# Kernel tuning notes

Hardware: AMD Instinct MI355X
Metric: run time of the kernel (lower is better)

The kernel has to match this reference:

```python
import jax, jax.numpy as jnp
import numpy as np

X_DIM, R_DIM, U_DIM, V_DIM, H_DIM = 64, 64, 64, 64, 128


def setup_inputs() -> dict:
    key = jax.random.key(0)
    k1, k2, k3, k4, k5 = jax.random.split(key, 5)
    n, i, j = 8, 32, 32
    r = jax.random.normal(k1, (n, i, j, R_DIM), dtype=jnp.float32)
    u = jax.random.normal(k2, (n, R_DIM, U_DIM, V_DIM), dtype=jnp.float32)
    v = jax.random.normal(k3, (n, i, j, V_DIM), dtype=jnp.float32)
    # xavier_uniform scaling: gain=1, fan computed over last two dims per torch default
    def xavier(k, shape):
        fan_in, fan_out = shape[-1], shape[-2]
        # torch xavier on >2D tensor: fan_in = shape[1]*prod(shape[2:]), fan_out = shape[0]*prod(shape[2:])
        rf = int(np.prod(shape[2:])) if len(shape) > 2 else 1
        fi = shape[1] * rf
        fo = shape[0] * rf
        bound = float(np.sqrt(6.0 / (fi + fo)))
        return jax.random.uniform(k, shape, dtype=jnp.float32, minval=-bound, maxval=bound)
    w1 = xavier(k4, (R_DIM, U_DIM, V_DIM, H_DIM))
    w2 = xavier(k5, (X_DIM, R_DIM, H_DIM))
    return {"r": r, "u": u, "v": v, "w1": w1, "w2": w2}


def reference(r, u, v, w1, w2):
    # contract w1 with u over (u_dim, v_dim) -> per-batch tensor a[n, r, v', h]
    # original: einsum('ruvh,nruv,nijv->nijrh')
    a = jnp.einsum('ruvh,nruv->nrvh', w1, u)          # contract u axis; v survives? no:
    # Careful: in 'ruvh,nruv,nijv->nijrh', v is contracted across all three.
    # Do it in two GEMM-friendly steps: first contract u-axis, keeping v.
    # a: [n, r, v, h] (contracted only over u)
    a = jnp.einsum('ruvh,nruv->nrvh', w1, u)
    # then contract v with v-tensor: [n,i,j,v] x [n,r,v,h] -> [n,i,j,r,h]
    x = jax.nn.relu(jnp.einsum('nijv,nrvh->nijrh', v, a))
    # second einsum: 'xrh,nijr,nijrh->nijx'
    # fuse r-weighting into x first (elementwise over r), then contract (r,h) with w2
    out = jnp.einsum('xrh,nijrh->nijx', w2, x * r[..., None])
    return out
```

## Files before the change

kernel.cpp:

```cpp
#include <hip/hip_runtime.h>
#include <hip/hip_bf16.h>

#define RD 64
#define UD 64
#define VD 64
#define HD 128
#define XD 64
#define NB 8
#define SITES 1024

typedef float f32x4 __attribute__((ext_vector_type(4)));
typedef __bf16 bf16x4 __attribute__((ext_vector_type(4)));
typedef __bf16 bf16x8 __attribute__((ext_vector_type(8)));
typedef unsigned int u32x4 __attribute__((ext_vector_type(4)));
typedef unsigned short u16;

__device__ __forceinline__ void gload_lds16(const void* g, void* l) {
  __builtin_amdgcn_global_load_lds((const __attribute__((address_space(1))) void*)g,
                                   (__attribute__((address_space(3))) void*)l, 16, 0, 0);
}

__global__ void kprep_w2(const float* __restrict__ w2, u16* __restrict__ w2t) {
  int b = blockIdx.x;
  int rr = b >> 2, qq = b & 3;
  int t = threadIdx.x;
  for (int i = 0; i < 8; ++i) {
    int idx = qq * 2048 + i * 256 + t;
    int x = idx >> 7, h = idx & 127;
    float val = w2[((size_t)x * RD + rr) * HD + h];
    __hip_bfloat16 hv = __float2bfloat16(val);
    w2t[((size_t)rr * XD + x) * HD + h] = *(u16*)&hv;
  }
}

__global__ void kprep_r(const float* __restrict__ r, float* __restrict__ rt) {
  __shared__ float tl[64][68];
  int b = blockIdx.x;
  int n = b >> 4, sb = (b & 15) * 64;
  int t = threadIdx.x;
  for (int i = 0; i < 4; ++i) {
    int flat = i * 256 + t;
    int s = flat >> 4, ch = flat & 15;
    f32x4 d = *(const f32x4*)(r + ((size_t)(n * SITES + sb + s) * RD + ch * 4));
    *(f32x4*)&tl[s][ch * 4] = d;
  }
  __syncthreads();
  for (int i = 0; i < 4; ++i) {
    int flat = i * 256 + t;
    int rr = flat >> 4, ch = flat & 15;
    f32x4 o;
    o.x = tl[ch * 4 + 0][rr];
    o.y = tl[ch * 4 + 1][rr];
    o.z = tl[ch * 4 + 2][rr];
    o.w = tl[ch * 4 + 3][rr];
    *(f32x4*)(rt + ((size_t)(n * RD + rr) * SITES + sb + ch * 4)) = o;
  }
}

__global__ __launch_bounds__(256) void k_a(const float* __restrict__ w1,
                                           const float* __restrict__ uT,
                                           u16* __restrict__ at) {
  __shared__ float w1s[2][64][32];
  __shared__ float us[2][8][64];
  __shared__ __align__(16) u16 tile[32][72];
  int b = blockIdx.x;
  int rr = b >> 2, hb = b & 3;
  int t = threadIdx.x;
  int v = t >> 2, hs = t & 3;
  int un_ = t >> 5, uidx = t & 31;
  float acc[8][8];
#pragma unroll
  for (int i = 0; i < 8; i++)
#pragma unroll
    for (int j = 0; j < 8; j++) acc[i][j] = 0.f;

  f32x4 pw[2][2];
  float2 pu[2];
  auto issue = [&](int uu, int rs) {
    const float* gp = w1 + (((size_t)(rr * UD + uu) * VD + v) * HD + hb * 32 + hs * 8);
    pw[rs][0] = *(const f32x4*)gp;
    pw[rs][1] = *(const f32x4*)(gp + 4);
    pu[rs] = *(const float2*)(uT + (((size_t)(un_ * RD + rr) * UD + uu) * VD + uidx * 2));
  };
  auto commit = [&](int rs, int buf) {
    *(f32x4*)&w1s[buf][v][hs * 8] = pw[rs][0];
    *(f32x4*)&w1s[buf][v][hs * 8 + 4] = pw[rs][1];
    us[buf][un_][uidx * 2] = pu[rs].x;
    us[buf][un_][uidx * 2 + 1] = pu[rs].y;
  };
  issue(0, 0);
  issue(1, 1);
  commit(0, 0);
  __syncthreads();
  for (int uu = 0; uu < 64; ++uu) {
    int bf = uu & 1;
    if (uu + 2 < 64) issue(uu + 2, bf);
    f32x4 c0 = *(const f32x4*)&w1s[bf][v][hs * 8];
    f32x4 c1 = *(const f32x4*)&w1s[bf][v][hs * 8 + 4];
    float wv[8] = {c0.x, c0.y, c0.z, c0.w, c1.x, c1.y, c1.z, c1.w};
    float uv[8];
#pragma unroll
    for (int nn = 0; nn < 8; nn++) uv[nn] = us[bf][nn][v];
#pragma unroll
    for (int nn = 0; nn < 8; nn++)
#pragma unroll
      for (int j = 0; j < 8; j++) acc[nn][j] += uv[nn] * wv[j];
    if (uu + 1 < 64) commit((uu + 1) & 1, 1 - bf);
    __syncthreads();
  }
  int hl = t >> 3, vbb = t & 7;
  for (int nn = 0; nn < 8; ++nn) {
    __syncthreads();
#pragma unroll
    for (int j = 0; j < 8; j++) {
      __hip_bfloat16 hv = __float2bfloat16(acc[nn][j]);
      tile[hs * 8 + j][v] = *(u16*)&hv;
    }
    __syncthreads();
    u32x4 blk = *(const u32x4*)&tile[hl][vbb * 8];
    int h = hb * 32 + hl;
    size_t off = ((size_t)(nn * RD + rr) * 8192) + (size_t)(h * 8 + (vbb ^ (h & 7))) * 8;
    *(u32x4*)(at + off) = blk;
  }
}

__global__ __launch_bounds__(256, 2) void k_main(const float* __restrict__ vin,
                                                 const u16* __restrict__ at,
                                                 const u16* __restrict__ w2t,
                                                 const float* __restrict__ rt,
                                                 float* __restrict__ out) {
  __shared__ __align__(16) char Alds[16384];
  __shared__ __align__(16) char Plds[128 * 272];
  int b = blockIdx.x;
  int rc = b & 7, st = (b >> 3) & 7, n = b >> 6;
  int t = threadIdx.x;
  int w = t >> 6, L = t & 63, q = L >> 4, c = L & 15;
  int g1m = w >> 1, g1n = w & 1;
  int g2m = w >> 1, g2x = w & 1;

  bf16x8 vf[4][2];
#pragma unroll
  for (int nt = 0; nt < 4; ++nt)
#pragma unroll
    for (int ks = 0; ks < 2; ++ks) {
      int s = g1n * 64 + nt * 16 + c;
      const float* vp = vin + ((size_t)(n * SITES + st * 128 + s) * VD + ks * 32 + q * 8);
      f32x4 a0 = *(const f32x4*)vp;
      f32x4 a1 = *(const f32x4*)(vp + 4);
      bf16x8 f;
      f[0] = (__bf16)a0.x; f[1] = (__bf16)a0.y; f[2] = (__bf16)a0.z; f[3] = (__bf16)a0.w;
      f[4] = (__bf16)a1.x; f[5] = (__bf16)a1.y; f[6] = (__bf16)a1.z; f[7] = (__bf16)a1.w;
      vf[nt][ks] = f;
    }

  f32x4 o[4][2];
#pragma unroll
  for (int i = 0; i < 4; i++)
#pragma unroll
    for (int j = 0; j < 2; j++) o[i][j] = (f32x4)0.f;

  for (int rr = rc * 8; rr < rc * 8 + 8; ++rr) {
    const char* abase = (const char*)at + (size_t)(n * RD + rr) * 16384;
#pragma unroll
    for (int i = 0; i < 4; i++)
      gload_lds16(abase + (size_t)(i * 256 + t) * 16, Alds + (i * 256 + t) * 16);

    u32x4 wraw[2][4];
#pragma unroll
    for (int xt = 0; xt < 2; ++xt)
#pragma unroll
      for (int k2 = 0; k2 < 4; ++k2) {
        int xg = g2x * 32 + xt * 16 + c;
        wraw[xt][k2] = *(const u32x4*)((const char*)w2t +
                        (((size_t)(rr * XD + xg)) * HD + k2 * 32 + q * 8) * 2);
      }
    float rsc[4];
#pragma unroll
    for (int nt = 0; nt < 4; ++nt)
      rsc[nt] = rt[(size_t)(n * RD + rr) * SITES + st * 128 + g1n * 64 + nt * 16 + c];

    __syncthreads();

    bf16x8 af[4][2];
#pragma unroll
    for (int mt = 0; mt < 4; ++mt)
#pragma unroll
      for (int ks = 0; ks < 2; ++ks) {
        int h = g1m * 64 + mt * 16 + c;
        int vb = ks * 4 + q;
        af[mt][ks] = *(const bf16x8*)(Alds + (size_t)(h * 8 + (vb ^ (h & 7))) * 16);
      }
    f32x4 cc[4][4];
#pragma unroll
    for (int mt = 0; mt < 4; ++mt)
#pragma unroll
      for (int nt = 0; nt < 4; ++nt) cc[mt][nt] = (f32x4)0.f;
#pragma unroll
    for (int ks = 0; ks < 2; ++ks)
#pragma unroll
      for (int mt = 0; mt < 4; ++mt)
#pragma unroll
        for (int nt = 0; nt < 4; ++nt)
          cc[mt][nt] = __builtin_amdgcn_mfma_f32_16x16x32_bf16(af[mt][ks], vf[nt][ks],
                                                               cc[mt][nt], 0, 0, 0);

#pragma unroll
    for (int mt = 0; mt < 4; ++mt)
#pragma unroll
      for (int nt = 0; nt < 4; ++nt) {
        float sc = rsc[nt];
        bf16x4 pv;
#pragma unroll
        for (int jj = 0; jj < 4; ++jj) {
          float x = cc[mt][nt][jj];
          x = x > 0.f ? x : 0.f;
          pv[jj] = (__bf16)(x * sc);
        }
        int s = g1n * 64 + nt * 16 + c;
        *(bf16x4*)(Plds + (size_t)s * 272 + (size_t)(g1m * 64 + mt * 16 + q * 4) * 2) = pv;
      }
    __syncthreads();

#pragma unroll
    for (int k2 = 0; k2 < 4; ++k2) {
      bf16x8 wf0 = __builtin_bit_cast(bf16x8, wraw[0][k2]);
      bf16x8 wf1 = __builtin_bit_cast(bf16x8, wraw[1][k2]);
#pragma unroll
      for (int mt = 0; mt < 4; ++mt) {
        int s = g2m * 64 + mt * 16 + c;
        bf16x8 pf = *(const bf16x8*)(Plds + (size_t)s * 272 + (size_t)(k2 * 32 + q * 8) * 2);
        o[mt][0] = __builtin_amdgcn_mfma_f32_16x16x32_bf16(pf, wf0, o[mt][0], 0, 0, 0);
        o[mt][1] = __builtin_amdgcn_mfma_f32_16x16x32_bf16(pf, wf1, o[mt][1], 0, 0, 0);
      }
    }
  }
#pragma unroll
  for (int mt = 0; mt < 4; ++mt)
#pragma unroll
    for (int xt = 0; xt < 2; ++xt)
#pragma unroll
      for (int jj = 0; jj < 4; ++jj) {
        int s = g2m * 64 + mt * 16 + q * 4 + jj;
        int x = g2x * 32 + xt * 16 + c;
        atomicAdd(out + ((size_t)(n * SITES + st * 128 + s) * XD + x), o[mt][xt][jj]);
      }
}

extern "C" void kernel_launch(void* const* d_in, const int* in_sizes, int n_in,
                              void* d_out, int out_size, void* d_ws, size_t ws_size,
                              hipStream_t stream) {
  const float* r  = (const float*)d_in[0];
  const float* u  = (const float*)d_in[1];
  const float* v  = (const float*)d_in[2];
  const float* w1 = (const float*)d_in[3];
  const float* w2 = (const float*)d_in[4];
  float* out = (float*)d_out;
  char* ws = (char*)d_ws;
  u16* at   = (u16*)(ws);
  u16* w2t  = (u16*)(ws + ((size_t)8 << 20));
  float* rt = (float*)(ws + ((size_t)9 << 20));

  hipMemsetAsync(d_out, 0, (size_t)out_size * sizeof(float), stream);
  hipLaunchKernelGGL(kprep_w2, dim3(256), dim3(256), 0, stream, w2, w2t);
  hipLaunchKernelGGL(kprep_r, dim3(128), dim3(256), 0, stream, r, rt);
  hipLaunchKernelGGL(k_a, dim3(256), dim3(256), 0, stream, w1, u, at);
  hipLaunchKernelGGL(k_main, dim3(512), dim3(256), 0, stream, v, at, w2t, rt, out);
}
```

Measured before the change: 304.6 us.

## Rewrite k_a without LDS staging and add u transpose prep kernel

Restructures the w1·u contraction kernel so each thread reads w1 and u straight from global memory instead of staging them through double-buffered shared memory with per-iteration barriers. A new kernel transposes u so that the 8 batch values for each (r,u,v) sit contiguously and can be read as vector loads. The grid is doubled to 512 blocks with a smaller per-thread accumulator, and the bf16 results are written as scattered 2-byte stores rather than through an LDS tile. This removes barrier stalls and adds occupancy, at the cost of an extra launch, extra workspace for the transposed u, and uncoalesced output stores. When the workspace is too small, a fallback path does strided scalar loads of u.

```diff
diff --git a/kernel.cpp b/kernel.cpp
--- a/kernel.cpp
+++ b/kernel.cpp
@@ -57,71 +57,65 @@
   }
 }
 
+__global__ void kprep_u(const float* __restrict__ u, float* __restrict__ ut) {
+  int f = blockIdx.x * 256 + threadIdx.x;
+  int nh = f & 1, v = (f >> 1) & 63, uu = (f >> 7) & 63, rr = f >> 13;
+  f32x4 o;
+#pragma unroll
+  for (int k = 0; k < 4; ++k)
+    o[k] = u[(((size_t)(nh * 4 + k) * RD + rr) * UD + uu) * VD + v];
+  *(f32x4*)(ut + (size_t)f * 4) = o;
+}
+
+template <bool USE_UT>
 __global__ __launch_bounds__(256) void k_a(const float* __restrict__ w1,
-                                           const float* __restrict__ uT,
+                                           const float* __restrict__ usrc,
                                            u16* __restrict__ at) {
-  __shared__ float w1s[2][64][32];
-  __shared__ float us[2][8][64];
-  __shared__ __align__(16) u16 tile[32][72];
-  int b = blockIdx.x;
-  int rr = b >> 2, hb = b & 3;
-  int t = threadIdx.x;
-  int v = t >> 2, hs = t & 3;
-  int un_ = t >> 5, uidx = t & 31;
-  float acc[8][8];
-#pragma unroll
-  for (int i = 0; i < 8; i++)
-#pragma unroll
-    for (int j = 0; j < 8; j++) acc[i][j] = 0.f;
-
-  f32x4 pw[2][2];
-  float2 pu[2];
-  auto issue = [&](int uu, int rs) {
-    const float* gp = w1 + (((size_t)(rr * UD + uu) * VD + v) * HD + hb * 32 + hs * 8);
-    pw[rs][0] = *(const f32x4*)gp;
-    pw[rs][1] = *(const f32x4*)(gp + 4);
-    pu[rs] = *(const float2*)(uT + (((size_t)(un_ * RD + rr) * UD + uu) * VD + uidx * 2));
-  };
-  auto commit = [&](int rs, int buf) {
-    *(f32x4*)&w1s[buf][v][hs * 8] = pw[rs][0];
-    *(f32x4*)&w1s[buf][v][hs * 8 + 4] = pw[rs][1];
-    us[buf][un_][uidx * 2] = pu[rs].x;
-    us[buf][un_][uidx * 2 + 1] = pu[rs].y;
-  };
-  issue(0, 0);
-  issue(1, 1);
-  commit(0, 0);
-  __syncthreads();
+  int b = blockIdx.x;
+  int rr = b >> 3, vh = (b >> 2) & 1, hb = b & 3;
+  int t = threadIdx.x;
+  int vl = t >> 3, hs = t & 7;
+  int v = vh * 32 + vl;
+  int h0 = hb * 32 + hs * 4;
+  const float* w1p = w1 + ((size_t)rr * UD * VD + v) * HD + h0;
+  const float* up = USE_UT ? (usrc + ((size_t)rr * UD * VD + v) * NB) : nullptr;
+
+  float acc[8][4];
+#pragma unroll
+  for (int n = 0; n < 8; ++n)
+#pragma unroll
+    for (int j = 0; j < 4; ++j) acc[n][j] = 0.f;
+
+#pragma unroll 4
   for (int uu = 0; uu < 64; ++uu) {
-    int bf = uu & 1;
-    if (uu + 2 < 64) issue(uu + 2, bf);
-    f32x4 c0 = *(const f32x4*)&w1s[bf][v][hs * 8];
-    f32x4 c1 = *(const f32x4*)&w1s[bf][v][hs * 8 + 4];
-    float wv[8] = {c0.x, c0.y, c0.z, c0.w, c1.x, c1.y, c1.z, c1.w};
-    float uv[8];
-#pragma unroll
-    for (int nn = 0; nn < 8; nn++) uv[nn] = us[bf][nn][v];
-#pragma unroll
-    for (int nn = 0; nn < 8; nn++)
-#pragma unroll
-      for (int j = 0; j < 8; j++) acc[nn][j] += uv[nn] * wv[j];
-    if (uu + 1 < 64) commit((uu + 1) & 1, 1 - bf);
-    __syncthreads();
-  }
-  int hl = t >> 3, vbb = t & 7;
-  for (int nn = 0; nn < 8; ++nn) {
-    __syncthreads();
-#pragma unroll
-    for (int j = 0; j < 8; j++) {
-      __hip_bfloat16 hv = __float2bfloat16(acc[nn][j]);
-      tile[hs * 8 + j][v] = *(u16*)&hv;
-    }
-    __syncthreads();
-    u32x4 blk = *(const u32x4*)&tile[hl][vbb * 8];
-    int h = hb * 32 + hl;
-    size_t off = ((size_t)(nn * RD + rr) * 8192) + (size_t)(h * 8 + (vbb ^ (h & 7))) * 8;
-    *(u32x4*)(at + off) = blk;
-  }
+    f32x4 wv = *(const f32x4*)(w1p + (size_t)uu * (VD * HD));
+    float un[8];
+    if (USE_UT) {
+      f32x4 a0 = *(const f32x4*)(up + (size_t)uu * (VD * NB));
+      f32x4 a1 = *(const f32x4*)(up + (size_t)uu * (VD * NB) + 4);
+      un[0] = a0.x; un[1] = a0.y; un[2] = a0.z; un[3] = a0.w;
+      un[4] = a1.x; un[5] = a1.y; un[6] = a1.z; un[7] = a1.w;
+    } else {
+#pragma unroll
+      for (int n = 0; n < 8; ++n)
+        un[n] = usrc[(((size_t)n * RD + rr) * UD + uu) * VD + v];
+    }
+#pragma unroll
+    for (int n = 0; n < 8; ++n)
+#pragma unroll
+      for (int j = 0; j < 4; ++j) acc[n][j] += un[n] * wv[j];
+  }
+
+  int vb = v >> 3, vlo = v & 7;
+#pragma unroll
+  for (int n = 0; n < 8; ++n)
+#pragma unroll
+    for (int j = 0; j < 4; ++j) {
+      int h = h0 + j;
+      __hip_bfloat16 hv = __float2bfloat16(acc[n][j]);
+      size_t off = ((size_t)(n * RD + rr) * 8192) + (size_t)(h * 8 + (vb ^ (h & 7))) * 8 + vlo;
+      at[off] = *(u16*)&hv;
+    }
 }
 
 __global__ __launch_bounds__(256, 2) void k_main(const float* __restrict__ vin,
@@ -259,10 +253,17 @@
   u16* at   = (u16*)(ws);
   u16* w2t  = (u16*)(ws + ((size_t)8 << 20));
   float* rt = (float*)(ws + ((size_t)9 << 20));
+  float* ut = (float*)(ws + ((size_t)11 << 20));
+  bool use_ut = ws_size >= ((size_t)19 << 20);
 
   hipMemsetAsync(d_out, 0, (size_t)out_size * sizeof(float), stream);
   hipLaunchKernelGGL(kprep_w2, dim3(256), dim3(256), 0, stream, w2, w2t);
   hipLaunchKernelGGL(kprep_r, dim3(128), dim3(256), 0, stream, r, rt);
-  hipLaunchKernelGGL(k_a, dim3(256), dim3(256), 0, stream, w1, u, at);
+  if (use_ut) {
+    hipLaunchKernelGGL(kprep_u, dim3(2048), dim3(256), 0, stream, u, ut);
+    hipLaunchKernelGGL((k_a<true>), dim3(512), dim3(256), 0, stream, w1, ut, at);
+  } else {
+    hipLaunchKernelGGL((k_a<false>), dim3(512), dim3(256), 0, stream, w1, u, at);
+  }
   hipLaunchKernelGGL(k_main, dim3(512), dim3(256), 0, stream, v, at, w2t, rt, out);
 }
```

Result: faster. 271.0 us (-11.1%).
